# Performance work log

Measured on AMD Instinct MI355X. Metric: run time of the kernel, lower is better.

The kernel has to match this reference:

```python
import jax, jax.numpy as jnp
import numpy as np
from jax.scipy.special import gammaln

# Static config (matches init_kwargs)
B, H, W = 64, 64, 64
CIN, COUT, K = 16, 32, 3
STRIDE = 1
CURV = 1.0            # manifold curvature c
CLAMP_F = 1.0         # clamping_factor
SMOOTH_F = 50.0       # smoothing_factor
EPS = 1e-7


def _log_beta_half(n):
    # log B(n/2, 1/2)
    return gammaln(n / 2.0) + gammaln(0.5) - gammaln((n + 1) / 2.0)


def setup_inputs() -> dict:
    key = jax.random.key(0)
    k1, k2, k3 = jax.random.split(key, 3)
    # inputs are Poincare-ball points: small norm keeps them well inside the ball
    x = jax.random.normal(k1, (B, H, W, CIN), dtype=jnp.float32) * 0.05
    n_in = K * K * CIN
    z = jax.random.normal(k2, (n_in, COUT), dtype=jnp.float32) * (1.0 / np.sqrt(n_in))
    r = jax.random.normal(k3, (COUT,), dtype=jnp.float32) * 0.01
    return {"x": x, "z": z, "r": r}


def reference(x, z, r):
    c = jnp.float32(CURV)
    sc = jnp.sqrt(c)
    kh = kw = K
    # ---- SAME padding with edge mode (stride 1 => pad K-1 total per dim) ----
    ph, pw = kh - 1, kw - 1
    pt, pb = ph // 2, ph - ph // 2
    pl, pr = pw // 2, pw - pw // 2
    xp = jnp.pad(x, ((0, 0), (pt, pb), (pl, pr), (0, 0)), mode='edge')
    # ---- im2col patch extraction: (B, H, W, CIN*K*K) with (C, kh, kw) channel order ----
    patches = jax.lax.conv_general_dilated_patches(
        xp, filter_shape=(kh, kw), window_strides=(STRIDE, STRIDE), padding='VALID',
        dimension_numbers=('NHWC', 'OIHW', 'NHWC'))
    p = patches.reshape(B, H, W, CIN, kh, kw).transpose(0, 1, 2, 4, 5, 3)
    p = p.reshape(-1, kh * kw * CIN)              # (N, K^2*CIN), concat order = (kh, kw, C)
    n_in = kh * kw * CIN
    # ---- beta-concatenation (HNN++): scale each block by B(n/2,1/2)/B(ni/2,1/2) ----
    ratio = jnp.exp(_log_beta_half(jnp.float32(n_in)) - _log_beta_half(jnp.float32(CIN))).astype(x.dtype)
    y = ratio * p
    # safety projection back into the ball
    yn = jnp.linalg.norm(y, axis=-1, keepdims=True)
    max_norm = (1.0 - 1e-5) / sc
    y = jnp.where(yn > max_norm, y * (max_norm / jnp.maximum(yn, EPS)), y)
    # ---- Poincare MLR (Shimizu et al. 2020, unidirectional) ----
    yn2 = jnp.sum(y * y, axis=-1, keepdims=True)            # (N,1)
    lam = 2.0 / jnp.maximum(1.0 - c * yn2, EPS)             # conformal factor
    zn = jnp.maximum(jnp.linalg.norm(z, axis=0, keepdims=True), EPS)  # (1,COUT)
    xz = y @ z                                              # (N,COUT)
    two_cr = 2.0 * sc * r                                   # (COUT,)
    arg = lam * sc * (xz / zn) * jnp.cosh(two_cr) - (lam - 1.0) * jnp.sinh(two_cr)
    v = (2.0 * zn / sc) * jnp.arcsinh(arg)                  # (N,COUT)
    # soft clamping (clamping_factor * smoothing * tanh(v/smoothing))
    v = CLAMP_F * SMOOTH_F * jnp.tanh(v / SMOOTH_F)
    # ---- Poincare FC output map: y_out = w / (1 + sqrt(1 + c||w||^2)) ----
    w = jnp.sinh(sc * v) / sc
    wn2 = c * jnp.sum(w * w, axis=-1, keepdims=True)
    out = w / (1.0 + jnp.sqrt(1.0 + wn2))
    return out.reshape(B, H, W, COUT)
```

## Files before the change

kernel.cpp:

```cpp
#include <hip/hip_runtime.h>
#include <cmath>

#define BB 64
#define HH 64
#define WW 64
#define CI 16
#define CO 32
#define NIN 144

typedef __attribute__((ext_vector_type(8)))  short s16x8;
typedef __attribute__((ext_vector_type(16))) float f32x16;

__device__ __forceinline__ unsigned pk_bf16(float a, float b) {
    unsigned ua = __float_as_uint(a);
    unsigned ub = __float_as_uint(b);
    ua = (ua + 0x7fffu + ((ua >> 16) & 1u)) >> 16;
    ub = (ub + 0x7fffu + ((ub >> 16) & 1u)) & 0xffff0000u;
    return ua | ub;
}

__global__ __launch_bounds__(256, 5) void hyp_fused(
        const float* __restrict__ x,
        const float* __restrict__ z,
        const float* __restrict__ r,
        float* __restrict__ out,
        float ratio, float ratio2) {
    __shared__ __align__(16) unsigned short xs[2][4][66][8];
    __shared__ __align__(16) unsigned zf[9][64][4];
    __shared__ float  qs[4][66];
    __shared__ float  tpart[8][32];
    __shared__ float2 lam2[128];
    __shared__ __align__(16) float pre4[32][4];

    const int tid  = threadIdx.x;
    const int lane = tid & 63;
    const int wv   = tid >> 6;

    const int bid = blockIdx.x;
    const int lid = ((bid & 7) << 8) | (bid >> 3);
    const int b   = lid >> 5;
    const int h   = (lid & 31) << 1;

    float rv = 0.f;
    if (tid < 32) rv = r[tid];

    const float* xb = x + (b << 16);

    for (int cell = tid; cell < 4 * 66; cell += 256) {
        int rr = cell / 66;
        int wi = cell - rr * 66;
        int gh = h - 1 + rr; gh = gh < 0 ? 0 : (gh > HH - 1 ? HH - 1 : gh);
        int gw = wi - 1;     gw = gw < 0 ? 0 : gw;
        gw = gw > WW - 1 ? WW - 1 : gw;
        const float4* src = (const float4*)(xb + ((gh << 6) + gw) * CI);
        float4 v0 = src[0], v1 = src[1], v2 = src[2], v3 = src[3];
        float q = 0.f;
        q = fmaf(v0.x, v0.x, q); q = fmaf(v0.y, v0.y, q);
        q = fmaf(v0.z, v0.z, q); q = fmaf(v0.w, v0.w, q);
        q = fmaf(v1.x, v1.x, q); q = fmaf(v1.y, v1.y, q);
        q = fmaf(v1.z, v1.z, q); q = fmaf(v1.w, v1.w, q);
        q = fmaf(v2.x, v2.x, q); q = fmaf(v2.y, v2.y, q);
        q = fmaf(v2.z, v2.z, q); q = fmaf(v2.w, v2.w, q);
        q = fmaf(v3.x, v3.x, q); q = fmaf(v3.y, v3.y, q);
        q = fmaf(v3.z, v3.z, q); q = fmaf(v3.w, v3.w, q);
        uint4 lo, hi4;
        lo.x  = pk_bf16(v0.x, v0.y);  lo.y  = pk_bf16(v0.z, v0.w);
        lo.z  = pk_bf16(v1.x, v1.y);  lo.w  = pk_bf16(v1.z, v1.w);
        hi4.x = pk_bf16(v2.x, v2.y);  hi4.y = pk_bf16(v2.z, v2.w);
        hi4.z = pk_bf16(v3.x, v3.y);  hi4.w = pk_bf16(v3.z, v3.w);
        *(uint4*)&xs[0][rr][wi][0] = lo;
        *(uint4*)&xs[1][rr][wi][0] = hi4;
        qs[rr][wi] = q;
    }

    {
        int ch = tid & 31;
        int p0 = tid >> 5;
        float sq = 0.f;
#pragma unroll
        for (int rep = 0; rep < 9; ++rep) {
            int k2 = rep * 8 + p0;
            float z0 = z[(k2 << 6) + ch];
            float z1 = z[(k2 << 6) + 32 + ch];
            sq = fmaf(z0, z0, fmaf(z1, z1, sq));
            int s  = k2 >> 3;
            int hi = (k2 >> 2) & 1;
            int j2 = k2 & 3;
            zf[s][ch | (hi << 5)][j2] = pk_bf16(ratio * z0, ratio * z1);
        }
        tpart[p0][ch] = sq;
    }
    __syncthreads();

    if (tid < 128) {
        int rr = tid >> 6, c = tid & 63;
        float s2 = 0.f;
#pragma unroll
        for (int kh = 0; kh < 3; ++kh)
#pragma unroll
            for (int kw = 0; kw < 3; ++kw)
                s2 += qs[rr + kh][c + kw];
        s2 *= ratio2;
        float yn = sqrtf(s2);
        float se = 1.0f;
        const float mn = 0.99999f;
        if (yn > mn) se = mn / fmaxf(yn, 1e-7f);
        float yn2 = s2 * se * se;
        float lam = 2.0f * __builtin_amdgcn_rcpf(fmaxf(1.0f - yn2, 1e-7f));
        lam2[tid] = make_float2(lam * se, lam - 1.0f);
    }
    if (tid < 32) {
        float s = tpart[0][tid];
#pragma unroll
        for (int p = 1; p < 8; ++p) s += tpart[p][tid];
        float zn = fmaxf(sqrtf(s), 1e-7f);
        float tc = 2.0f * rv;
        pre4[tid][0] = coshf(tc) / zn;
        pre4[tid][1] = sinhf(tc);
        pre4[tid][2] = 2.0f * zn;
    }

    const int px    = lane & 31;
    const int hi    = lane >> 5;
    const int rloc  = wv >> 1;
    const int cbase = (wv & 1) << 5;

    f32x16 acc = {};
#pragma unroll
    for (int s = 0; s < 9; ++s) {
        const int kh = s / 3, kw = s % 3;
        s16x8 afrag = *(const s16x8*)&zf[s][lane][0];
        s16x8 bfrag = *(const s16x8*)&xs[hi][rloc + kh][cbase + px + kw][0];
        acc = __builtin_amdgcn_mfma_f32_32x32x16_bf16(afrag, bfrag, acc, 0, 0, 0);
    }
    __syncthreads();

    float2 lm2 = lam2[(rloc << 6) + cbase + px];
    const float ls = lm2.x, lm = lm2.y;
    float wn2 = 0.f;
#pragma unroll
    for (int reg = 0; reg < 16; ++reg) {
        const int m = (reg & 3) + ((reg >> 2) << 3) + (hi << 2);
        float4 t4 = *(const float4*)&pre4[m][0];
        float arg = fmaf(ls * acc[reg], t4.x, -(lm * t4.y));
        float ax  = fabsf(arg);
        float v = copysignf(t4.z * __logf(ax + __builtin_amdgcn_sqrtf(fmaf(ax, ax, 1.f))), arg);
        float u = v * 0.02f;
        float qq = u * u;
        float t = v * fmaf(qq, fmaf(qq, 0.1333333f, -0.3333333f), 1.0f);
        float e = __expf(t);
        float w = 0.5f * (e - __builtin_amdgcn_rcpf(e));
        acc[reg] = w;
        wn2 = fmaf(w, w, wn2);
    }
    wn2 += __shfl_xor(wn2, 32);
    float inv = __builtin_amdgcn_rcpf(1.f + __builtin_amdgcn_sqrtf(1.f + wn2));

    float* op = out + ((((b << 6) + h + rloc) << 6) + cbase + px) * CO + (hi << 2);
#pragma unroll
    for (int q = 0; q < 4; ++q) {
        float4 o;
        o.x = acc[q * 4 + 0] * inv;
        o.y = acc[q * 4 + 1] * inv;
        o.z = acc[q * 4 + 2] * inv;
        o.w = acc[q * 4 + 3] * inv;
        *(float4*)(op + (q << 3)) = o;
    }
}

extern "C" void kernel_launch(void* const* d_in, const int* in_sizes, int n_in,
                              void* d_out, int out_size, void* d_ws, size_t ws_size,
                              hipStream_t stream) {
    const float* x = (const float*)d_in[0];
    const float* z = (const float*)d_in[1];
    const float* r = (const float*)d_in[2];
    float* out = (float*)d_out;

    double lb_n = lgamma(NIN / 2.0) + lgamma(0.5) - lgamma((NIN + 1) / 2.0);
    double lb_c = lgamma(CI  / 2.0) + lgamma(0.5) - lgamma((CI  + 1) / 2.0);
    float ratio = (float)exp(lb_n - lb_c);

    hyp_fused<<<BB * HH / 2, 256, 0, stream>>>(x, z, r, out, ratio, ratio * ratio);
}
```

Before: 22.57 us.

## Process four output rows per block, reusing z fragments across two MFMA tiles

Each block now covers four image rows instead of two, and each wave computes two 32x32 MFMA tiles that share the same z fragment. The grid is halved, so the per-block z load, norm reduction and halo overhead are amortized over twice the output. The asinh log is changed to log2 with ln2 folded into the per-channel scale, and bf16 packing now uses the HIP intrinsic. The cost is more registers (two accumulators) and a lower occupancy hint in launch bounds.

```diff
diff --git a/kernel.cpp b/kernel.cpp
--- a/kernel.cpp
+++ b/kernel.cpp
@@ -1,5 +1,7 @@
 #include <hip/hip_runtime.h>
+#include <hip/hip_bf16.h>
 #include <cmath>
+#include <cstring>
 
 #define BB 64
 #define HH 64
@@ -11,25 +13,24 @@
 typedef __attribute__((ext_vector_type(8)))  short s16x8;
 typedef __attribute__((ext_vector_type(16))) float f32x16;
 
-__device__ __forceinline__ unsigned pk_bf16(float a, float b) {
-    unsigned ua = __float_as_uint(a);
-    unsigned ub = __float_as_uint(b);
-    ua = (ua + 0x7fffu + ((ua >> 16) & 1u)) >> 16;
-    ub = (ub + 0x7fffu + ((ub >> 16) & 1u)) & 0xffff0000u;
-    return ua | ub;
+__device__ __forceinline__ unsigned pk2(float a, float b) {
+    __hip_bfloat162 h = __float22bfloat162_rn(make_float2(a, b));
+    unsigned u;
+    memcpy(&u, &h, sizeof(u));
+    return u;
 }
 
-__global__ __launch_bounds__(256, 5) void hyp_fused(
+__global__ __launch_bounds__(256, 4) void hyp_fused(
         const float* __restrict__ x,
         const float* __restrict__ z,
         const float* __restrict__ r,
         float* __restrict__ out,
         float ratio, float ratio2) {
-    __shared__ __align__(16) unsigned short xs[2][4][66][8];
+    __shared__ __align__(16) unsigned short xs[2][6][66][8];
     __shared__ __align__(16) unsigned zf[9][64][4];
-    __shared__ float  qs[4][66];
+    __shared__ float  qs[6][66];
     __shared__ float  tpart[8][32];
-    __shared__ float2 lam2[128];
+    __shared__ float2 lam2[256];
     __shared__ __align__(16) float pre4[32][4];
 
     const int tid  = threadIdx.x;
@@ -37,21 +38,20 @@
     const int wv   = tid >> 6;
 
     const int bid = blockIdx.x;
-    const int lid = ((bid & 7) << 8) | (bid >> 3);
-    const int b   = lid >> 5;
-    const int h   = (lid & 31) << 1;
+    const int lid = ((bid & 7) << 7) | (bid >> 3);
+    const int b   = lid >> 4;
+    const int h   = (lid & 15) << 2;
 
     float rv = 0.f;
     if (tid < 32) rv = r[tid];
 
     const float* xb = x + (b << 16);
 
-    for (int cell = tid; cell < 4 * 66; cell += 256) {
+    for (int cell = tid; cell < 6 * 66; cell += 256) {
         int rr = cell / 66;
         int wi = cell - rr * 66;
         int gh = h - 1 + rr; gh = gh < 0 ? 0 : (gh > HH - 1 ? HH - 1 : gh);
-        int gw = wi - 1;     gw = gw < 0 ? 0 : gw;
-        gw = gw > WW - 1 ? WW - 1 : gw;
+        int gw = wi - 1;     gw = gw < 0 ? 0 : (gw > WW - 1 ? WW - 1 : gw);
         const float4* src = (const float4*)(xb + ((gh << 6) + gw) * CI);
         float4 v0 = src[0], v1 = src[1], v2 = src[2], v3 = src[3];
         float q = 0.f;
@@ -64,10 +64,10 @@
         q = fmaf(v3.x, v3.x, q); q = fmaf(v3.y, v3.y, q);
         q = fmaf(v3.z, v3.z, q); q = fmaf(v3.w, v3.w, q);
         uint4 lo, hi4;
-        lo.x  = pk_bf16(v0.x, v0.y);  lo.y  = pk_bf16(v0.z, v0.w);
-        lo.z  = pk_bf16(v1.x, v1.y);  lo.w  = pk_bf16(v1.z, v1.w);
-        hi4.x = pk_bf16(v2.x, v2.y);  hi4.y = pk_bf16(v2.z, v2.w);
-        hi4.z = pk_bf16(v3.x, v3.y);  hi4.w = pk_bf16(v3.z, v3.w);
+        lo.x  = pk2(v0.x, v0.y);  lo.y  = pk2(v0.z, v0.w);
+        lo.z  = pk2(v1.x, v1.y);  lo.w  = pk2(v1.z, v1.w);
+        hi4.x = pk2(v2.x, v2.y);  hi4.y = pk2(v2.z, v2.w);
+        hi4.z = pk2(v3.x, v3.y);  hi4.w = pk2(v3.z, v3.w);
         *(uint4*)&xs[0][rr][wi][0] = lo;
         *(uint4*)&xs[1][rr][wi][0] = hi4;
         qs[rr][wi] = q;
@@ -86,13 +86,13 @@
             int s  = k2 >> 3;
             int hi = (k2 >> 2) & 1;
             int j2 = k2 & 3;
-            zf[s][ch | (hi << 5)][j2] = pk_bf16(ratio * z0, ratio * z1);
+            zf[s][ch | (hi << 5)][j2] = pk2(ratio * z0, ratio * z1);
         }
         tpart[p0][ch] = sq;
     }
     __syncthreads();
 
-    if (tid < 128) {
+    {
         int rr = tid >> 6, c = tid & 63;
         float s2 = 0.f;
 #pragma unroll
@@ -117,54 +117,74 @@
         float tc = 2.0f * rv;
         pre4[tid][0] = coshf(tc) / zn;
         pre4[tid][1] = sinhf(tc);
-        pre4[tid][2] = 2.0f * zn;
+        pre4[tid][2] = 2.0f * zn * 0.69314718f;
     }
 
     const int px    = lane & 31;
     const int hi    = lane >> 5;
     const int rloc  = wv >> 1;
-    const int cbase = (wv & 1) << 5;
-
-    f32x16 acc = {};
+    const int cb    = (wv & 1) << 5;
+
+    f32x16 accA = {}, accB = {};
 #pragma unroll
     for (int s = 0; s < 9; ++s) {
         const int kh = s / 3, kw = s % 3;
         s16x8 afrag = *(const s16x8*)&zf[s][lane][0];
-        s16x8 bfrag = *(const s16x8*)&xs[hi][rloc + kh][cbase + px + kw][0];
-        acc = __builtin_amdgcn_mfma_f32_32x32x16_bf16(afrag, bfrag, acc, 0, 0, 0);
+        s16x8 bfA = *(const s16x8*)&xs[hi][rloc + kh][cb + px + kw][0];
+        s16x8 bfB = *(const s16x8*)&xs[hi][rloc + 2 + kh][cb + px + kw][0];
+        accA = __builtin_amdgcn_mfma_f32_32x32x16_bf16(afrag, bfA, accA, 0, 0, 0);
+        accB = __builtin_amdgcn_mfma_f32_32x32x16_bf16(afrag, bfB, accB, 0, 0, 0);
     }
     __syncthreads();
 
-    float2 lm2 = lam2[(rloc << 6) + cbase + px];
-    const float ls = lm2.x, lm = lm2.y;
-    float wn2 = 0.f;
+    float2 lA = lam2[(rloc << 6) + cb + px];
+    float2 lB = lam2[((rloc + 2) << 6) + cb + px];
+    float wn2A = 0.f, wn2B = 0.f;
 #pragma unroll
     for (int reg = 0; reg < 16; ++reg) {
         const int m = (reg & 3) + ((reg >> 2) << 3) + (hi << 2);
         float4 t4 = *(const float4*)&pre4[m][0];
-        float arg = fmaf(ls * acc[reg], t4.x, -(lm * t4.y));
-        float ax  = fabsf(arg);
-        float v = copysignf(t4.z * __logf(ax + __builtin_amdgcn_sqrtf(fmaf(ax, ax, 1.f))), arg);
-        float u = v * 0.02f;
-        float qq = u * u;
-        float t = v * fmaf(qq, fmaf(qq, 0.1333333f, -0.3333333f), 1.0f);
-        float e = __expf(t);
-        float w = 0.5f * (e - __builtin_amdgcn_rcpf(e));
-        acc[reg] = w;
-        wn2 = fmaf(w, w, wn2);
-    }
-    wn2 += __shfl_xor(wn2, 32);
-    float inv = __builtin_amdgcn_rcpf(1.f + __builtin_amdgcn_sqrtf(1.f + wn2));
-
-    float* op = out + ((((b << 6) + h + rloc) << 6) + cbase + px) * CO + (hi << 2);
+        {
+            float arg = fmaf(lA.x * accA[reg], t4.x, -(lA.y * t4.y));
+            float ax  = fabsf(arg);
+            float v = copysignf(t4.z * __log2f(ax + __builtin_amdgcn_sqrtf(fmaf(ax, ax, 1.f))), arg);
+            float u = v * 0.02f;
+            float qq = u * u;
+            float t = v * fmaf(qq, fmaf(qq, 0.1333333f, -0.3333333f), 1.0f);
+            float e = __expf(t);
+            float w = 0.5f * (e - __builtin_amdgcn_rcpf(e));
+            accA[reg] = w;
+            wn2A = fmaf(w, w, wn2A);
+        }
+        {
+            float arg = fmaf(lB.x * accB[reg], t4.x, -(lB.y * t4.y));
+            float ax  = fabsf(arg);
+            float v = copysignf(t4.z * __log2f(ax + __builtin_amdgcn_sqrtf(fmaf(ax, ax, 1.f))), arg);
+            float u = v * 0.02f;
+            float qq = u * u;
+            float t = v * fmaf(qq, fmaf(qq, 0.1333333f, -0.3333333f), 1.0f);
+            float e = __expf(t);
+            float w = 0.5f * (e - __builtin_amdgcn_rcpf(e));
+            accB[reg] = w;
+            wn2B = fmaf(w, w, wn2B);
+        }
+    }
+    wn2A += __shfl_xor(wn2A, 32);
+    wn2B += __shfl_xor(wn2B, 32);
+    float invA = __builtin_amdgcn_rcpf(1.f + __builtin_amdgcn_sqrtf(1.f + wn2A));
+    float invB = __builtin_amdgcn_rcpf(1.f + __builtin_amdgcn_sqrtf(1.f + wn2B));
+
+    float* opA = out + ((((b << 6) + h + rloc)     << 6) + cb + px) * CO + (hi << 2);
+    float* opB = out + ((((b << 6) + h + rloc + 2) << 6) + cb + px) * CO + (hi << 2);
 #pragma unroll
     for (int q = 0; q < 4; ++q) {
-        float4 o;
-        o.x = acc[q * 4 + 0] * inv;
-        o.y = acc[q * 4 + 1] * inv;
-        o.z = acc[q * 4 + 2] * inv;
-        o.w = acc[q * 4 + 3] * inv;
-        *(float4*)(op + (q << 3)) = o;
+        float4 oA, oB;
+        oA.x = accA[q * 4 + 0] * invA; oA.y = accA[q * 4 + 1] * invA;
+        oA.z = accA[q * 4 + 2] * invA; oA.w = accA[q * 4 + 3] * invA;
+        oB.x = accB[q * 4 + 0] * invB; oB.y = accB[q * 4 + 1] * invB;
+        oB.z = accB[q * 4 + 2] * invB; oB.w = accB[q * 4 + 3] * invB;
+        *(float4*)(opA + (q << 3)) = oA;
+        *(float4*)(opB + (q << 3)) = oB;
     }
 }
 
@@ -180,5 +200,5 @@
     double lb_c = lgamma(CI  / 2.0) + lgamma(0.5) - lgamma((CI  + 1) / 2.0);
     float ratio = (float)exp(lb_n - lb_c);
 
-    hyp_fused<<<BB * HH / 2, 256, 0, stream>>>(x, z, r, out, ratio, ratio * ratio);
+    hyp_fused<<<BB * HH / 4, 256, 0, stream>>>(x, z, r, out, ratio, ratio * ratio);
 }
```

Result: faster. 20.44 us (-9.4%).
